# Kernel tuning notes

Measured on AMD Instinct MI355X. Metric: run time of the kernel, lower is better.

## Reference

```python
import jax, jax.numpy as jnp
import numpy as np

D_MODEL = 256; N_HEADS = 8; N_LEVELS = 4; N_POINTS = 4; D_FFN = 1024
BS = 8; NQ = 100; NKPT = 17
LEVEL_SHAPES = [(160, 160), (80, 80), (40, 40), (20, 20)]  # (H, W) per level
LEN_V = sum(h * w for h, w in LEVEL_SHAPES)  # 34000


def layer_norm(x, g, b, eps=1e-5):
    m = x.mean(-1, keepdims=True)
    v = ((x - m) ** 2).mean(-1, keepdims=True)
    return (x - m) * jax.lax.rsqrt(v + eps) * g + b


def mha(q, k, v, Wqkv, bqkv, Wo, bo):
    # torch nn.MultiheadAttention, batch_first, eval mode (no dropout)
    d = q.shape[-1]; dh = d // N_HEADS
    def proj(x, W, b):
        return (x @ W.T + b).reshape(*x.shape[:-1], N_HEADS, dh)
    qp = proj(q, Wqkv[:d], bqkv[:d])
    kp = proj(k, Wqkv[d:2 * d], bqkv[d:2 * d])
    vp = proj(v, Wqkv[2 * d:], bqkv[2 * d:])
    att = jnp.einsum('bqhd,bkhd->bhqk', qp, kp) / jnp.sqrt(jnp.asarray(dh, q.dtype))
    att = jax.nn.softmax(att, -1)
    out = jnp.einsum('bhqk,bkhd->bqhd', att, vp).reshape(q.shape)
    return out @ Wo.T + bo


def bilinear_sample(val, loc, h, w):
    # val: (B, H, h*w, Dh); loc: (B, Lq, H, P, 2) normalized to [0,1]
    # matches F.grid_sample(align_corners=False, padding_mode='zeros') on grid 2*loc-1
    B, Lq, H, P, _ = loc.shape
    px = loc[..., 0] * w - 0.5
    py = loc[..., 1] * h - 0.5
    x0f = jnp.floor(px); y0f = jnp.floor(py)
    lx = px - x0f; ly = py - y0f
    x0 = x0f.astype(jnp.int32); y0 = y0f.astype(jnp.int32)
    out = jnp.zeros((B, H, Lq, P, val.shape[-1]), val.dtype)
    for dx, dy, wt in ((0, 0, (1 - lx) * (1 - ly)), (1, 0, lx * (1 - ly)),
                       (0, 1, (1 - lx) * ly), (1, 1, lx * ly)):
        xi = x0 + dx; yi = y0 + dy
        valid = ((xi >= 0) & (xi < w) & (yi >= 0) & (yi < h)).astype(val.dtype)
        idx = jnp.clip(yi, 0, h - 1) * w + jnp.clip(xi, 0, w - 1)  # (B,Lq,H,P)
        idx = idx.transpose(0, 2, 1, 3).reshape(B, H, Lq * P)
        g = jnp.take_along_axis(val, idx[..., None], axis=2).reshape(B, H, Lq, P, -1)
        out = out + g * (wt * valid).transpose(0, 2, 1, 3)[..., None]
    return out  # (B, H, Lq, P, Dh)


def ms_deform_attn(query, ref_points, memory, off_W, off_b, aw_W, aw_b,
                   val_W, val_b, outp_W, outp_b):
    B, Lq, _ = query.shape
    dh = D_MODEL // N_HEADS
    value = (memory @ val_W.T + val_b).reshape(B, LEN_V, N_HEADS, dh)
    off = (query @ off_W.T + off_b).reshape(B, Lq, N_HEADS, N_LEVELS, N_POINTS, 2)
    aw = (query @ aw_W.T + aw_b).reshape(B, Lq, N_HEADS, N_LEVELS * N_POINTS)
    aw = jax.nn.softmax(aw, -1).reshape(B, Lq, N_HEADS, N_LEVELS, N_POINTS)
    normalizer = jnp.array([[w, h] for h, w in LEVEL_SHAPES], dtype=query.dtype)  # (L,2) as (W,H)
    loc = ref_points[:, :, None, :, None, :] + off / normalizer[None, None, None, :, None, :]
    out = jnp.zeros((B, Lq, N_HEADS, dh), query.dtype)
    start = 0
    for l, (h, w) in enumerate(LEVEL_SHAPES):
        vl = value[:, start:start + h * w].transpose(0, 2, 1, 3)  # (B,H,hw,Dh)
        s = bilinear_sample(vl, loc[:, :, :, l], h, w)            # (B,H,Lq,P,Dh)
        out = out + jnp.einsum('bhqpd,bqhp->bqhd', s, aw[:, :, :, l])
        start += h * w
    return out.reshape(B, Lq, D_MODEL) @ outp_W.T + outp_b


def setup_inputs() -> dict:
    key = jax.random.key(0)
    ks = iter(jax.random.split(key, 40))
    d = D_MODEL
    def w(shape, s=0.02):
        return jax.random.normal(next(ks), shape, jnp.float32) * s
    inp = {
        'tgt_pose': jax.random.normal(next(ks), (BS, NQ, NKPT, d), jnp.float32),
        'tgt_pose_query_pos': jax.random.normal(next(ks), (BS, NQ, NKPT, d), jnp.float32),
        'tgt_pose_reference_points': jax.random.uniform(next(ks), (BS, NQ * NKPT, N_LEVELS, 2), jnp.float32),
        'memory': jax.random.normal(next(ks), (BS, LEN_V, d), jnp.float32),
        'win_Wqkv': w((3 * d, d)), 'win_bqkv': jnp.zeros((3 * d,), jnp.float32),
        'win_Wo': w((d, d)), 'win_bo': jnp.zeros((d,), jnp.float32),
        'win_ng': jnp.ones((d,), jnp.float32), 'win_nb': jnp.zeros((d,), jnp.float32),
        'acr_Wqkv': w((3 * d, d)), 'acr_bqkv': jnp.zeros((3 * d,), jnp.float32),
        'acr_Wo': w((d, d)), 'acr_bo': jnp.zeros((d,), jnp.float32),
        'acr_ng': jnp.ones((d,), jnp.float32), 'acr_nb': jnp.zeros((d,), jnp.float32),
        'off_W': w((N_HEADS * N_LEVELS * N_POINTS * 2, d)),
        'off_b': jax.random.uniform(next(ks), (N_HEADS * N_LEVELS * N_POINTS * 2,), jnp.float32, -1.0, 1.0),
        'aw_W': w((N_HEADS * N_LEVELS * N_POINTS, d)), 'aw_b': jnp.zeros((N_HEADS * N_LEVELS * N_POINTS,), jnp.float32),
        'val_W': w((d, d)), 'val_b': jnp.zeros((d,), jnp.float32),
        'outp_W': w((d, d)), 'outp_b': jnp.zeros((d,), jnp.float32),
        'gate_W': w((2 * d, 2 * d)), 'gate_b': jnp.zeros((2 * d,), jnp.float32),
        'gate_ng': jnp.ones((d,), jnp.float32), 'gate_nb': jnp.zeros((d,), jnp.float32),
        'ffn_W1': w((D_FFN, d)), 'ffn_b1': jnp.zeros((D_FFN,), jnp.float32),
        'ffn_W2': w((d, D_FFN)), 'ffn_b2': jnp.zeros((d,), jnp.float32),
        'n2_g': jnp.ones((d,), jnp.float32), 'n2_b': jnp.zeros((d,), jnp.float32),
        'memory_spatial_shapes': jnp.array(LEVEL_SHAPES, jnp.int32),
    }
    return inp


def reference(tgt_pose, tgt_pose_query_pos, tgt_pose_reference_points, memory,
              win_Wqkv, win_bqkv, win_Wo, win_bo, win_ng, win_nb,
              acr_Wqkv, acr_bqkv, acr_Wo, acr_bo, acr_ng, acr_nb,
              off_W, off_b, aw_W, aw_b, val_W, val_b, outp_W, outp_b,
              gate_W, gate_b, gate_ng, gate_nb,
              ffn_W1, ffn_b1, ffn_W2, ffn_b2, n2_g, n2_b,
              memory_spatial_shapes):
    bs, nq, K, d = tgt_pose.shape
    # with_pos_embed mutates tgt_pose in place in the torch code -> residual includes pos
    tgt = tgt_pose + tgt_pose_query_pos
    # within-attention over keypoints of each query
    x = tgt.reshape(bs * nq, K, d)
    t2 = mha(x, x, x, win_Wqkv, win_bqkv, win_Wo, win_bo).reshape(bs, nq, K, d)
    tgt = layer_norm(tgt + t2, win_ng, win_nb)
    # across-attention over queries for each keypoint
    xk = tgt.transpose(0, 2, 1, 3).reshape(bs * K, nq, d)
    t2 = mha(xk, xk, xk, acr_Wqkv, acr_bqkv, acr_Wo, acr_bo)
    tgt = layer_norm(xk + t2, acr_ng, acr_nb).reshape(bs, K, nq, d).transpose(0, 2, 1, 3)
    # second in-place pos add before deformable cross-attn (also feeds gateway)
    tgt_q = tgt + tgt_pose_query_pos
    t2 = ms_deform_attn(tgt_q.reshape(bs, nq * K, d), tgt_pose_reference_points, memory,
                        off_W, off_b, aw_W, aw_b, val_W, val_b, outp_W, outp_b)
    t2 = t2.reshape(bs, nq, K, d)
    # Gate
    g = jax.nn.sigmoid(jnp.concatenate([tgt_q, t2], -1) @ gate_W.T + gate_b)
    g1, g2 = jnp.split(g, 2, -1)
    tgt = layer_norm(g1 * tgt_q + g2 * t2, gate_ng, gate_nb)
    # FFN
    h = jax.nn.relu(tgt @ ffn_W1.T + ffn_b1)
    tgt = tgt + h @ ffn_W2.T + ffn_b2
    tgt = layer_norm(jnp.clip(tgt, -65504.0, 65504.0), n2_g, n2_b)
    return tgt
```

## Files before the change

kernel.cpp:

```cpp
#include <hip/hip_runtime.h>
#include <hip/hip_bf16.h>

#define NH 8
#define BS_ 8
#define NQ_ 100
#define NK_ 17
#define LQ 1700
#define T_TOK 13600
#define LEN_VV 34000

typedef __attribute__((ext_vector_type(8))) short short8v;
typedef __attribute__((ext_vector_type(8))) __bf16 bf16x8;
typedef __attribute__((ext_vector_type(4))) float f32x4;

__device__ __forceinline__ float wave_sum(float v){
#pragma unroll
  for (int m = 32; m; m >>= 1) v += __shfl_xor(v, m, 64);
  return v;
}
__device__ __forceinline__ short f2bf(float f){
  __hip_bfloat16 h = __float2bfloat16(f);
  return *reinterpret_cast<short*>(&h);
}
__device__ __forceinline__ float bf2f(short s){
  return __uint_as_float(((uint)(unsigned short)s) << 16);
}

template<int EPI, int ADDA, int SWZ>
__global__ __launch_bounds__(256) void mgemm_k(const float* __restrict__ A,
                                               const float* __restrict__ A2,
                                               const float* __restrict__ W,
                                               const float* __restrict__ bias,
                                               __hip_bfloat16* __restrict__ Cb,
                                               int M, int N, int K, int nbx){
  __shared__ short sh[128 * 136];
  short* As = sh;
  short* Ws = sh + 128 * 64;
  int j;
  if (SWZ){
    int total = gridDim.x;
    int q = total >> 3, r = total & 7;
    int x = blockIdx.x & 7, k = blockIdx.x >> 3;
    j = (x < r) ? x * (q + 1) + k : r * (q + 1) + (x - r) * q + k;
  } else {
    j = blockIdx.x;
  }
  const int tid = threadIdx.x;
  const int bm = (j / nbx) * 128, bn = (j % nbx) * 128;
  const int wave = tid >> 6, lane = tid & 63;
  const int wm = (wave >> 1) * 64, wn = (wave & 1) * 64;
  const int s = tid & 7;
  const int row0 = tid >> 3;
  f32x4 acc[4][4] = {};
  const int lrow = lane & 15, lk = lane >> 4;

  float4 ra[8], rw[8];
#pragma unroll
  for (int i = 0; i < 4; i++){
    int row = row0 + i * 32;
    int gr = bm + row;
    float4 z = make_float4(0.f, 0.f, 0.f, 0.f);
    if (gr < M){
      const float* p = A + (size_t)gr * K + s * 8;
      float4 x0 = ((const float4*)p)[0], x1 = ((const float4*)p)[1];
      if (ADDA){
        const float* q2 = A2 + (size_t)gr * K + s * 8;
        float4 y0 = ((const float4*)q2)[0], y1 = ((const float4*)q2)[1];
        x0.x+=y0.x; x0.y+=y0.y; x0.z+=y0.z; x0.w+=y0.w;
        x1.x+=y1.x; x1.y+=y1.y; x1.z+=y1.z; x1.w+=y1.w;
      }
      ra[2 * i] = x0; ra[2 * i + 1] = x1;
    } else { ra[2 * i] = z; ra[2 * i + 1] = z; }
    const float* q = W + (size_t)(bn + row) * K + s * 8;
    rw[2 * i] = ((const float4*)q)[0]; rw[2 * i + 1] = ((const float4*)q)[1];
  }

  for (int k0 = 0; k0 < K; k0 += 64){
#pragma unroll
    for (int i = 0; i < 4; i++){
      int row = row0 + i * 32;
      int sw = ((s ^ (row & 7)) << 3) + row * 64;
      float4 a0 = ra[2 * i], a1 = ra[2 * i + 1];
      short8v v;
      v[0]=f2bf(a0.x); v[1]=f2bf(a0.y); v[2]=f2bf(a0.z); v[3]=f2bf(a0.w);
      v[4]=f2bf(a1.x); v[5]=f2bf(a1.y); v[6]=f2bf(a1.z); v[7]=f2bf(a1.w);
      *(short8v*)&As[sw] = v;
      a0 = rw[2 * i]; a1 = rw[2 * i + 1];
      short8v u;
      u[0]=f2bf(a0.x); u[1]=f2bf(a0.y); u[2]=f2bf(a0.z); u[3]=f2bf(a0.w);
      u[4]=f2bf(a1.x); u[5]=f2bf(a1.y); u[6]=f2bf(a1.z); u[7]=f2bf(a1.w);
      *(short8v*)&Ws[sw] = u;
    }
    __syncthreads();
    if (k0 + 64 < K){
#pragma unroll
      for (int i = 0; i < 4; i++){
        int row = row0 + i * 32;
        int gr = bm + row;
        float4 z = make_float4(0.f, 0.f, 0.f, 0.f);
        if (gr < M){
          const float* p = A + (size_t)gr * K + k0 + 64 + s * 8;
          float4 x0 = ((const float4*)p)[0], x1 = ((const float4*)p)[1];
          if (ADDA){
            const float* q2 = A2 + (size_t)gr * K + k0 + 64 + s * 8;
            float4 y0 = ((const float4*)q2)[0], y1 = ((const float4*)q2)[1];
            x0.x+=y0.x; x0.y+=y0.y; x0.z+=y0.z; x0.w+=y0.w;
            x1.x+=y1.x; x1.y+=y1.y; x1.z+=y1.z; x1.w+=y1.w;
          }
          ra[2 * i] = x0; ra[2 * i + 1] = x1;
        } else { ra[2 * i] = z; ra[2 * i + 1] = z; }
        const float* q = W + (size_t)(bn + row) * K + k0 + 64 + s * 8;
        rw[2 * i] = ((const float4*)q)[0]; rw[2 * i + 1] = ((const float4*)q)[1];
      }
    }
#pragma unroll
    for (int ks = 0; ks < 2; ks++){
      short8v af[4], bw[4];
      int slot = ks * 4 + lk;
#pragma unroll
      for (int m = 0; m < 4; m++){
        int r = wm + m * 16 + lrow;
        af[m] = *(const short8v*)&As[r * 64 + ((slot ^ (r & 7)) << 3)];
      }
#pragma unroll
      for (int n = 0; n < 4; n++){
        int r = wn + n * 16 + lrow;
        bw[n] = *(const short8v*)&Ws[r * 64 + ((slot ^ (r & 7)) << 3)];
      }
#pragma unroll
      for (int m = 0; m < 4; m++)
#pragma unroll
        for (int n = 0; n < 4; n++)
          acc[m][n] = __builtin_amdgcn_mfma_f32_16x16x32_bf16(
              __builtin_bit_cast(bf16x8, af[m]),
              __builtin_bit_cast(bf16x8, bw[n]), acc[m][n], 0, 0, 0);
    }
    __syncthreads();
  }
  const int STR = 136;
#pragma unroll
  for (int n = 0; n < 4; n++){
    int col = wn + n * 16 + lrow;
    float bsv = bias[bn + col];
#pragma unroll
    for (int m = 0; m < 4; m++){
#pragma unroll
      for (int i = 0; i < 4; i++){
        int row = wm + m * 16 + lk * 4 + i;
        float c = acc[m][n][i] + bsv;
        if (EPI == 1) c = fmaxf(c, 0.f);
        sh[row * STR + col] = f2bf(c);
      }
    }
  }
  __syncthreads();
#pragma unroll
  for (int it = 0; it < 8; it++){
    int r = it * 16 + (tid >> 4);
    int chunk = tid & 15;
    if (bm + r < M){
      uint4 v = *(const uint4*)((const char*)sh + r * 272 + chunk * 16);
      *(uint4*)((char*)Cb + ((size_t)(bm + r) * N + bn) * 2 + chunk * 16) = v;
    }
  }
}

template<int EPI, int OUTB, int INB, int DUALA>
__global__ __launch_bounds__(256) void g64_k(const void* __restrict__ Av,
                                             const void* __restrict__ A1v,
                                             const float* __restrict__ W0,
                                             const float* __restrict__ W1,
                                             int NSPLIT,
                                             const float* __restrict__ bias0,
                                             const float* __restrict__ bias1,
                                             const float* __restrict__ RES,
                                             float* __restrict__ Cf,
                                             __hip_bfloat16* __restrict__ Cb,
                                             int M, int N, int K, int sA){
  __shared__ short sh64[2 * 64 * 64];
  short* As = sh64;
  short* Ws = sh64 + 64 * 64;
  const int tid = threadIdx.x;
  const int bn = blockIdx.x * 64, bm = blockIdx.y * 64;
  const int wave = tid >> 6, lane = tid & 63;
  const int wm = (wave >> 1) * 32, wn = (wave & 1) * 32;
  const int s = tid & 7, row0 = tid >> 3;
  const int lrow = lane & 15, lk = lane >> 4;
  f32x4 acc[2][2] = {};

  for (int k0 = 0; k0 < K; k0 += 64){
#pragma unroll
    for (int i = 0; i < 2; i++){
      int row = row0 + i * 32;
      int sw = ((s ^ (row & 7)) << 3) + row * 64;
      short8v v = {};
      int gr = bm + row;
      if (gr < M){
        if (INB){
          v = *(const short8v*)((const short*)Av + (size_t)gr * sA + k0 + s * 8);
        } else {
          const float* Ap;
          if (DUALA) Ap = (k0 < 256) ? (const float*)Av + (size_t)gr * 256 + k0
                                     : (const float*)A1v + (size_t)gr * 256 + (k0 - 256);
          else Ap = (const float*)Av + (size_t)gr * sA + k0;
          float4 a0 = ((const float4*)(Ap + s * 8))[0];
          float4 a1 = ((const float4*)(Ap + s * 8))[1];
          v[0]=f2bf(a0.x); v[1]=f2bf(a0.y); v[2]=f2bf(a0.z); v[3]=f2bf(a0.w);
          v[4]=f2bf(a1.x); v[5]=f2bf(a1.y); v[6]=f2bf(a1.z); v[7]=f2bf(a1.w);
        }
      }
      *(short8v*)&As[sw] = v;
      int wr = bn + row;
      const float* Wp = (wr < NSPLIT) ? W0 + (size_t)wr * K + k0
                                      : W1 + (size_t)(wr - NSPLIT) * K + k0;
      float4 b0 = ((const float4*)(Wp + s * 8))[0];
      float4 b1 = ((const float4*)(Wp + s * 8))[1];
      short8v u;
      u[0]=f2bf(b0.x); u[1]=f2bf(b0.y); u[2]=f2bf(b0.z); u[3]=f2bf(b0.w);
      u[4]=f2bf(b1.x); u[5]=f2bf(b1.y); u[6]=f2bf(b1.z); u[7]=f2bf(b1.w);
      *(short8v*)&Ws[sw] = u;
    }
    __syncthreads();
#pragma unroll
    for (int ks = 0; ks < 2; ks++){
      int slot = ks * 4 + lk;
      short8v af[2], bw[2];
#pragma unroll
      for (int m = 0; m < 2; m++){
        int r = wm + m * 16 + lrow;
        af[m] = *(const short8v*)&As[r * 64 + ((slot ^ (r & 7)) << 3)];
      }
#pragma unroll
      for (int n = 0; n < 2; n++){
        int r = wn + n * 16 + lrow;
        bw[n] = *(const short8v*)&Ws[r * 64 + ((slot ^ (r & 7)) << 3)];
      }
#pragma unroll
      for (int m = 0; m < 2; m++)
#pragma unroll
        for (int n = 0; n < 2; n++)
          acc[m][n] = __builtin_amdgcn_mfma_f32_16x16x32_bf16(
              __builtin_bit_cast(bf16x8, af[m]),
              __builtin_bit_cast(bf16x8, bw[n]), acc[m][n], 0, 0, 0);
    }
    __syncthreads();
  }
  if (OUTB){
    const int STR = 72;
#pragma unroll
    for (int n = 0; n < 2; n++){
      int col = wn + n * 16 + lrow;
      int gc = bn + col;
      float bsv = (gc < NSPLIT) ? bias0[gc] : bias1[gc - NSPLIT];
#pragma unroll
      for (int m = 0; m < 2; m++){
#pragma unroll
        for (int i = 0; i < 4; i++){
          int row = wm + m * 16 + lk * 4 + i;
          float c = acc[m][n][i] + bsv;
          if (EPI == 1) c = fmaxf(c, 0.f);
          if (EPI == 2) c = 1.f / (1.f + expf(-c));
          sh64[row * STR + col] = f2bf(c);
        }
      }
    }
    __syncthreads();
#pragma unroll
    for (int it = 0; it < 2; it++){
      int r = it * 32 + (tid >> 3);
      int chunk = tid & 7;
      if (bm + r < M){
        uint4 v = *(const uint4*)((const char*)sh64 + r * 144 + chunk * 16);
        *(uint4*)((char*)Cb + ((size_t)(bm + r) * N + bn) * 2 + chunk * 16) = v;
      }
    }
  } else {
#pragma unroll
    for (int n = 0; n < 2; n++){
      int gc = bn + wn + n * 16 + lrow;
      float bsv = (gc < NSPLIT) ? bias0[gc] : bias1[gc - NSPLIT];
#pragma unroll
      for (int m = 0; m < 2; m++){
#pragma unroll
        for (int i = 0; i < 4; i++){
          int row = bm + wm + m * 16 + lk * 4 + i;
          if (row >= M) continue;
          float c = acc[m][n][i] + bsv;
          if (EPI == 1) c = fmaxf(c, 0.f);
          if (EPI == 2) c = 1.f / (1.f + expf(-c));
          if (EPI == 3) c += RES[(size_t)row * N + gc];
          Cf[(size_t)row * N + gc] = c;
        }
      }
    }
  }
}

template<int SITE>
__global__ __launch_bounds__(512) void gln_k(const short* __restrict__ Abf,
                                             const float* __restrict__ W,
                                             const float* __restrict__ bias,
                                             const float* __restrict__ r0,
                                             const float* __restrict__ r1,
                                             const float* __restrict__ g,
                                             const float* __restrict__ be,
                                             float* __restrict__ out,
                                             int M, int K){
  __shared__ short As[64 * 64];
  __shared__ short Ws[256 * 64];
  __shared__ float part[64][4][2];
  __shared__ float stats[64][2];
  const int tid = threadIdx.x;
  const int bm = blockIdx.x * 64;
  const int wave = tid >> 6, lane = tid & 63;
  const int wm = (wave >> 2) * 32, wn = (wave & 3) * 64;
  const int s = tid & 7, row0 = tid >> 3;
  const int lrow = lane & 15, lk = lane >> 4;
  f32x4 acc[2][4] = {};

  short8v pa = {};
  { int gr = bm + row0; if (gr < M) pa = *(const short8v*)(Abf + (size_t)gr * K + s * 8); }
  float4 pw[8];
#pragma unroll
  for (int i = 0; i < 4; i++){
    const float* wp = W + (size_t)(row0 + i * 64) * K + s * 8;
    pw[2 * i] = ((const float4*)wp)[0]; pw[2 * i + 1] = ((const float4*)wp)[1];
  }

  for (int k0 = 0; k0 < K; k0 += 64){
    *(short8v*)&As[row0 * 64 + ((s ^ (row0 & 7)) << 3)] = pa;
#pragma unroll
    for (int i = 0; i < 4; i++){
      int row = row0 + i * 64;
      float4 b0 = pw[2 * i], b1 = pw[2 * i + 1];
      short8v u;
      u[0]=f2bf(b0.x); u[1]=f2bf(b0.y); u[2]=f2bf(b0.z); u[3]=f2bf(b0.w);
      u[4]=f2bf(b1.x); u[5]=f2bf(b1.y); u[6]=f2bf(b1.z); u[7]=f2bf(b1.w);
      *(short8v*)&Ws[row * 64 + ((s ^ (row & 7)) << 3)] = u;
    }
    __syncthreads();
    if (k0 + 64 < K){
      int gr = bm + row0;
      pa = (short8v){};
      if (gr < M) pa = *(const short8v*)(Abf + (size_t)gr * K + k0 + 64 + s * 8);
#pragma unroll
      for (int i = 0; i < 4; i++){
        const float* wp = W + (size_t)(row0 + i * 64) * K + k0 + 64 + s * 8;
        pw[2 * i] = ((const float4*)wp)[0]; pw[2 * i + 1] = ((const float4*)wp)[1];
      }
    }
#pragma unroll
    for (int ks = 0; ks < 2; ks++){
      int slot = ks * 4 + lk;
      short8v af[2], bw[4];
#pragma unroll
      for (int m = 0; m < 2; m++){
        int r = wm + m * 16 + lrow;
        af[m] = *(const short8v*)&As[r * 64 + ((slot ^ (r & 7)) << 3)];
      }
#pragma unroll
      for (int n = 0; n < 4; n++){
        int r = wn + n * 16 + lrow;
        bw[n] = *(const short8v*)&Ws[r * 64 + ((slot ^ (r & 7)) << 3)];
      }
#pragma unroll
      for (int m = 0; m < 2; m++)
#pragma unroll
        for (int n = 0; n < 4; n++)
          acc[m][n] = __builtin_amdgcn_mfma_f32_16x16x32_bf16(
              __builtin_bit_cast(bf16x8, af[m]),
              __builtin_bit_cast(bf16x8, bw[n]), acc[m][n], 0, 0, 0);
    }
    __syncthreads();
  }

#pragma unroll
  for (int m = 0; m < 2; m++){
#pragma unroll
    for (int i = 0; i < 4; i++){
      int row = wm + m * 16 + lk * 4 + i;
      int grow = bm + row;
      float s1 = 0.f, s2 = 0.f;
      if (grow < M){
#pragma unroll
        for (int n = 0; n < 4; n++){
          int col = wn + n * 16 + lrow;
          float x = acc[m][n][i] + bias[col] + r0[(size_t)grow * 256 + col];
          if (SITE == 0) x += r1[(size_t)grow * 256 + col];
          if (SITE == 2) x = fminf(fmaxf(x, -65504.f), 65504.f);
          acc[m][n][i] = x;
          s1 += x; s2 += x * x;
        }
      }
#pragma unroll
      for (int msk = 1; msk <= 8; msk <<= 1){
        s1 += __shfl_xor(s1, msk, 64);
        s2 += __shfl_xor(s2, msk, 64);
      }
      if (lrow == 0){ part[row][wave & 3][0] = s1; part[row][wave & 3][1] = s2; }
    }
  }
  __syncthreads();
  if (tid < 64){
    float s1 = part[tid][0][0] + part[tid][1][0] + part[tid][2][0] + part[tid][3][0];
    float s2 = part[tid][0][1] + part[tid][1][1] + part[tid][2][1] + part[tid][3][1];
    float mean = s1 * (1.f / 256.f);
    float var = s2 * (1.f / 256.f) - mean * mean;
    stats[tid][0] = mean;
    stats[tid][1] = rsqrtf(fmaxf(var, 0.f) + 1e-5f);
  }
  __syncthreads();
#pragma unroll
  for (int m = 0; m < 2; m++){
#pragma unroll
    for (int i = 0; i < 4; i++){
      int row = wm + m * 16 + lk * 4 + i;
      int grow = bm + row;
      if (grow >= M) continue;
      float mean = stats[row][0], rstd = stats[row][1];
      size_t orow = grow;
      if (SITE == 0){
        int bi = grow / LQ; int rem = grow % LQ; int q = rem / NK_; int kk = rem % NK_;
        orow = (size_t)bi * LQ + kk * NQ_ + q;
      }
      if (SITE == 1){
        int bi = grow / LQ; int rem = grow % LQ; int kk = rem / NQ_; int q = rem % NQ_;
        orow = (size_t)bi * LQ + q * NK_ + kk;
      }
#pragma unroll
      for (int n = 0; n < 4; n++){
        int col = wn + n * 16 + lrow;
        float o = (acc[m][n][i] - mean) * rstd * g[col] + be[col];
        if (SITE == 1) o += r1[orow * 256 + col];
        out[orow * 256 + col] = o;
      }
    }
  }
}

template<int TP, int NSPL>
__global__ __launch_bounds__(256) void mha_mfma_k(const short* __restrict__ qkv,
                                                  __hip_bfloat16* __restrict__ out, int S){
  constexpr int MT = TP / 16;
  constexpr int KSTEPS = (TP + 31) / 32;
  constexpr int KS32 = KSTEPS * 32;
  constexpr int VSTRB = (KS32 == 128) ? 256 : 128;
  constexpr int CH = (MT + NSPL - 1) / NSPL;
  __shared__ short QK[2][TP][64];
  __shared__ short Vt[2][32][VSTRB / 2];
  __shared__ float Sc[2][16][128];
  __shared__ float rinv[2][16];

  const int tid = threadIdx.x;
  const int bid = blockIdx.x;
  const int batch = bid / (4 * NSPL);
  const int rem = bid % (4 * NSPL);
  const int hp = rem / NSPL;
  const int half = rem % NSPL;
  const int mtlo = half * CH;
  const int mthi = (mtlo + CH < MT) ? (mtlo + CH) : MT;
  const int wave = tid >> 6, lane = tid & 63;
  const int hh = wave >> 1, wsub = wave & 1;
  const int lrow = lane & 15, lk = lane >> 4;
  const float scale = 0.17677669529663687f;
  const size_t qbase = (size_t)batch * S * 768;

  for (int idx = tid; idx < 2 * TP * 4; idx += 256){
    int h2 = idx >= TP * 4;
    int rm = idx - h2 * TP * 4;
    int j = rm >> 2, s = rm & 3;
    int h = hp * 2 + h2;
    short8v qv = {}, kv = {};
    if (j < S){
      const short* p = qkv + qbase + (size_t)j * 768 + h * 32 + s * 8;
      qv = *(const short8v*)p;
      kv = *(const short8v*)(p + 256);
    }
    *(short8v*)&QK[h2][j][(s ^ (j & 7)) << 3] = qv;
    *(short8v*)&QK[h2][j][((s + 4) ^ (j & 7)) << 3] = kv;
  }
  for (int idx = tid; idx < 2 * KS32 * 4; idx += 256){
    int h2 = idx >= KS32 * 4;
    int rm = idx - h2 * KS32 * 4;
    int j = rm >> 2, e8 = rm & 3;
    int h = hp * 2 + h2;
    short8v v = {};
    if (j < S) v = *(const short8v*)(qkv + qbase + (size_t)j * 768 + h * 32 + 512 + e8 * 8);
#pragma unroll
    for (int c = 0; c < 8; c++){
      int e = e8 * 8 + c;
      char* pb = (char*)&Vt[h2][0][0] + e * VSTRB + (((j >> 3) ^ (e & 7)) << 4) + ((j & 7) << 1);
      *(short*)pb = v[c];
    }
  }
  __syncthreads();

  for (int mt = mtlo; mt < mthi; mt++){
    for (int nt = wsub; nt < MT; nt += 2){
      int ar = mt * 16 + lrow;
      short8v aq = *(const short8v*)&QK[hh][ar][(lk ^ (ar & 7)) << 3];
      int br = nt * 16 + lrow;
      short8v bk = *(const short8v*)&QK[hh][br][((lk + 4) ^ (br & 7)) << 3];
      f32x4 z = {};
      f32x4 d = __builtin_amdgcn_mfma_f32_16x16x32_bf16(
          __builtin_bit_cast(bf16x8, aq), __builtin_bit_cast(bf16x8, bk), z, 0, 0, 0);
#pragma unroll
      for (int i = 0; i < 4; i++){
        int rr = lk * 4 + i;
        int c = nt * 16 + lrow;
        Sc[hh][rr][(((c >> 2) ^ (rr & 7)) << 2) + (c & 3)] = d[i] * scale;
      }
    }
    __syncthreads();
    if (wsub == 0){
      int rr = lane >> 2, p = lane & 3;
      int grow = mt * 16 + rr;
      int Seff = (grow < S) ? S : 0;
      float mx = -1e30f;
#pragma unroll
      for (int m = 0; m < KSTEPS; m++){
        int j = p + 4 * m;
#pragma unroll
        for (int hf = 0; hf < 2; hf++){
          int ls = 2 * j + hf;
          float4 v = *(const float4*)&Sc[hh][rr][(ls ^ (rr & 7)) << 2];
          int c0 = ls * 4;
          mx = fmaxf(mx, (c0 + 0 < Seff) ? v.x : -1e30f);
          mx = fmaxf(mx, (c0 + 1 < Seff) ? v.y : -1e30f);
          mx = fmaxf(mx, (c0 + 2 < Seff) ? v.z : -1e30f);
          mx = fmaxf(mx, (c0 + 3 < Seff) ? v.w : -1e30f);
        }
      }
      mx = fmaxf(mx, __shfl_xor(mx, 1, 64));
      mx = fmaxf(mx, __shfl_xor(mx, 2, 64));
      float sum = 0.f;
#pragma unroll
      for (int m = 0; m < KSTEPS; m++){
        int j = p + 4 * m;
        float ev[8];
#pragma unroll
        for (int hf = 0; hf < 2; hf++){
          int ls = 2 * j + hf;
          float4 v = *(const float4*)&Sc[hh][rr][(ls ^ (rr & 7)) << 2];
          int c0 = ls * 4;
          ev[hf * 4 + 0] = (c0 + 0 < Seff) ? __expf(v.x - mx) : 0.f;
          ev[hf * 4 + 1] = (c0 + 1 < Seff) ? __expf(v.y - mx) : 0.f;
          ev[hf * 4 + 2] = (c0 + 2 < Seff) ? __expf(v.z - mx) : 0.f;
          ev[hf * 4 + 3] = (c0 + 3 < Seff) ? __expf(v.w - mx) : 0.f;
        }
        short8v pb;
#pragma unroll
        for (int q2 = 0; q2 < 8; q2++){ pb[q2] = f2bf(ev[q2]); sum += ev[q2]; }
        *(short8v*)((char*)&Sc[hh][rr][0] + ((j ^ (rr & 7)) << 4)) = pb;
      }
      sum += __shfl_xor(sum, 1, 64);
      sum += __shfl_xor(sum, 2, 64);
      if (p == 0) rinv[hh][rr] = (sum > 0.f) ? 1.f / sum : 0.f;
    }
    __syncthreads();
    {
      int nt2 = wsub;
      f32x4 acc = {};
#pragma unroll
      for (int ks = 0; ks < KSTEPS; ks++){
        int slot = ks * 4 + lk;
        short8v ap = *(const short8v*)((const char*)&Sc[hh][lrow][0] + ((slot ^ (lrow & 7)) << 4));
        int e = nt2 * 16 + lrow;
        short8v bv = *(const short8v*)((const char*)&Vt[hh][0][0] + e * VSTRB + ((slot ^ (e & 7)) << 4));
        acc = __builtin_amdgcn_mfma_f32_16x16x32_bf16(
            __builtin_bit_cast(bf16x8, ap), __builtin_bit_cast(bf16x8, bv), acc, 0, 0, 0);
      }
      int h = hp * 2 + hh;
#pragma unroll
      for (int i = 0; i < 4; i++){
        int row = mt * 16 + lk * 4 + i;
        if (row < S){
          float rv = rinv[hh][lk * 4 + i];
          out[((size_t)batch * S + row) * 256 + h * 32 + nt2 * 16 + lrow] =
              __float2bfloat16(acc[i] * rv);
        }
      }
    }
    __syncthreads();
  }
}

__global__ __launch_bounds__(64) void gate_ln_k(const short* __restrict__ G,
                                                const float* __restrict__ aq,
                                                const float* __restrict__ t2,
                                                const float* __restrict__ g,
                                                const float* __restrict__ be,
                                                float* __restrict__ out){
  int r = blockIdx.x;
  int lane = threadIdx.x;
  const short* gp = G + (size_t)r * 512 + lane * 4;
  float g1v[4], g2v[4];
#pragma unroll
  for (int i = 0; i < 4; i++){ g1v[i] = bf2f(gp[i]); g2v[i] = bf2f(gp[256 + i]); }
  float4 xa = *(const float4*)(aq + (size_t)r * 256 + lane * 4);
  float4 xt = *(const float4*)(t2 + (size_t)r * 256 + lane * 4);
  float x[4] = { g1v[0] * xa.x + g2v[0] * xt.x, g1v[1] * xa.y + g2v[1] * xt.y,
                 g1v[2] * xa.z + g2v[2] * xt.z, g1v[3] * xa.w + g2v[3] * xt.w };
  float s = x[0] + x[1] + x[2] + x[3];
  s = wave_sum(s);
  float mean = s * (1.f / 256.f);
  float sq = 0.f;
#pragma unroll
  for (int i = 0; i < 4; i++){ float d = x[i] - mean; sq += d * d; }
  float var = wave_sum(sq) * (1.f / 256.f);
  float rstd = rsqrtf(var + 1e-5f);
  float4 gg = *(const float4*)(g + lane * 4);
  float4 bb = *(const float4*)(be + lane * 4);
  float4 o;
  o.x = (x[0] - mean) * rstd * gg.x + bb.x;
  o.y = (x[1] - mean) * rstd * gg.y + bb.y;
  o.z = (x[2] - mean) * rstd * gg.z + bb.z;
  o.w = (x[3] - mean) * rstd * gg.w + bb.w;
  *(float4*)(out + (size_t)r * 256 + lane * 4) = o;
}

__global__ __launch_bounds__(256) void deform_k(const __hip_bfloat16* __restrict__ val,
                                                const float* __restrict__ offaw,
                                                const float* __restrict__ ref,
                                                unsigned int* __restrict__ outb){
  __shared__ uint2 meta[32][16][4];
  const int tid = threadIdx.x;
  const int t0 = blockIdx.x * 4;
  {
    int g = tid >> 3;
    int pair = tid & 7;
    int lt = g >> 3, h = g & 7;
    int t = t0 + lt;
    int b = t / LQ;
    int p0 = pair * 2;
    int l = p0 >> 2;
    const int starts[4] = {0, 25600, 32000, 33600};
    const int HS[4] = {160, 80, 40, 20};
    int w = HS[l];
    const float* ap = offaw + (size_t)t * 384 + 256 + h * 16;
    float a0 = ap[p0];
    float a1 = ap[p0 + 1];
    float mx = fmaxf(a0, a1);
#pragma unroll
    for (int m = 1; m <= 4; m <<= 1) mx = fmaxf(mx, __shfl_xor(mx, m, 64));
    float e0 = expf(a0 - mx), e1 = expf(a1 - mx);
    float s = e0 + e1;
#pragma unroll
    for (int m = 1; m <= 4; m <<= 1) s += __shfl_xor(s, m, 64);
    float inv = 1.f / s;
    float rx = ref[((size_t)t * 4 + l) * 2 + 0];
    float ry = ref[((size_t)t * 4 + l) * 2 + 1];
    float4 ov = *(const float4*)(offaw + (size_t)t * 384 + h * 32 + l * 8 + p0 * 2);
    int vbase = (b * LEN_VV + starts[l]) * 128 + h * 16;
#pragma unroll
    for (int pp = 0; pp < 2; pp++){
      float wgt = (pp ? e1 : e0) * inv;
      float px = rx * w + (pp ? ov.z : ov.x) - 0.5f;
      float py = ry * w + (pp ? ov.w : ov.y) - 0.5f;
      float x0f = floorf(px), y0f = floorf(py);
      float lx = px - x0f, ly = py - y0f;
      int x0 = (int)x0f, y0 = (int)y0f;
#pragma unroll
      for (int c = 0; c < 4; c++){
        int dx = c & 1, dy = c >> 1;
        int xi = x0 + dx, yi = y0 + dy;
        bool ok = (xi >= 0) & (xi < w) & (yi >= 0) & (yi < w);
        float cw = ok ? wgt * (dx ? lx : 1.f - lx) * (dy ? ly : 1.f - ly) : 0.f;
        uint idx = ok ? (uint)(vbase + (yi * w + xi) * 128) : 0u;
        uint2 m2; m2.x = idx; m2.y = __float_as_uint(cw);
        meta[g][p0 + pp][c] = m2;
      }
    }
  }
  __syncthreads();
  const uint2* V2 = (const uint2*)val;
  int sg = tid >> 3, lane8 = tid & 7;
  int lt = sg >> 3, h = sg & 7;
  int t = t0 + lt;
  float a0 = 0.f, a1 = 0.f, a2 = 0.f, a3 = 0.f;
#pragma unroll 4
  for (int c = 0; c < 64; c++){
    uint2 mw = meta[sg][c >> 2][c & 3];
    float wv = __uint_as_float(mw.y);
    uint2 v = V2[(size_t)(mw.x >> 1) + lane8];
    a0 += wv * __uint_as_float(v.x << 16);
    a1 += wv * __uint_as_float(v.x & 0xffff0000u);
    a2 += wv * __uint_as_float(v.y << 16);
    a3 += wv * __uint_as_float(v.y & 0xffff0000u);
  }
  uint2 u;
  u.x = ((uint)(unsigned short)f2bf(a1) << 16) | (uint)(unsigned short)f2bf(a0);
  u.y = ((uint)(unsigned short)f2bf(a3) << 16) | (uint)(unsigned short)f2bf(a2);
  ((uint2*)outb)[((size_t)t * 256 + h * 32) / 4 + lane8] = u;
}

extern "C" void kernel_launch(void* const* d_in, const int* in_sizes, int n_in,
                              void* d_out, int out_size, void* d_ws, size_t ws_size,
                              hipStream_t stream){
  const float* tgt_pose = (const float*)d_in[0];
  const float* qpos     = (const float*)d_in[1];
  const float* refp     = (const float*)d_in[2];
  const float* memory   = (const float*)d_in[3];
  const float* win_Wqkv = (const float*)d_in[4];
  const float* win_bqkv = (const float*)d_in[5];
  const float* win_Wo   = (const float*)d_in[6];
  const float* win_bo   = (const float*)d_in[7];
  const float* win_ng   = (const float*)d_in[8];
  const float* win_nb   = (const float*)d_in[9];
  const float* acr_Wqkv = (const float*)d_in[10];
  const float* acr_bqkv = (const float*)d_in[11];
  const float* acr_Wo   = (const float*)d_in[12];
  const float* acr_bo   = (const float*)d_in[13];
  const float* acr_ng   = (const float*)d_in[14];
  const float* acr_nb   = (const float*)d_in[15];
  const float* off_W    = (const float*)d_in[16];
  const float* off_b    = (const float*)d_in[17];
  const float* aw_W     = (const float*)d_in[18];
  const float* aw_b     = (const float*)d_in[19];
  const float* val_W    = (const float*)d_in[20];
  const float* val_b    = (const float*)d_in[21];
  const float* outp_W   = (const float*)d_in[22];
  const float* outp_b   = (const float*)d_in[23];
  const float* gate_W   = (const float*)d_in[24];
  const float* gate_b   = (const float*)d_in[25];
  const float* gate_ng  = (const float*)d_in[26];
  const float* gate_nb  = (const float*)d_in[27];
  const float* ffn_W1   = (const float*)d_in[28];
  const float* ffn_b1   = (const float*)d_in[29];
  const float* ffn_W2   = (const float*)d_in[30];
  const float* ffn_b2   = (const float*)d_in[31];
  const float* n2_g     = (const float*)d_in[32];
  const float* n2_b     = (const float*)d_in[33];

  float* out = (float*)d_out;
  char* ws = (char*)d_ws;
  const size_t TB = (size_t)T_TOK * 256 * 4;
  float* B0 = (float*)(ws);
  float* B1 = (float*)(ws + TB);
  float* B2 = (float*)(ws + 2 * TB);
  float* B3 = (float*)(ws + 3 * TB);
  char* p = ws + 4 * TB;
  short* Qb = (short*)p;                 p += (size_t)T_TOK * 768 * 2;
  short* ABF = (short*)p;                p += (size_t)T_TOK * 256 * 2;
  float* OFFAW = (float*)p;              p += (size_t)T_TOK * 384 * 4;
  short* Gb = (short*)p;                 p += (size_t)T_TOK * 512 * 2;
  char* Vregion = p;
  __hip_bfloat16* V = (__hip_bfloat16*)Vregion;
  short* FF = (short*)Vregion;

  const int GM128 = (T_TOK + 127) / 128;
  const int GM64  = (T_TOK + 63) / 64;
  const int BIG = 1 << 30;

  mgemm_k<0,0,1><<<2 * 2125, 256, 0, stream>>>(memory, nullptr, val_W, val_b, V, BS_ * LEN_VV, 256, 256, 2);
  mgemm_k<0,1,0><<<6 * GM128, 256, 0, stream>>>(tgt_pose, qpos, win_Wqkv, win_bqkv, (__hip_bfloat16*)Qb, T_TOK, 768, 256, 6);
  mha_mfma_k<32,1><<<800 * 4, 256, 0, stream>>>(Qb, (__hip_bfloat16*)ABF, 17);
  gln_k<0><<<GM64, 512, 0, stream>>>(ABF, win_Wo, win_bo, tgt_pose, qpos, win_ng, win_nb, B1, T_TOK, 256);
  mgemm_k<0,0,0><<<6 * GM128, 256, 0, stream>>>(B1, nullptr, acr_Wqkv, acr_bqkv, (__hip_bfloat16*)Qb, T_TOK, 768, 256, 6);
  mha_mfma_k<112,2><<<136 * 8, 256, 0, stream>>>(Qb, (__hip_bfloat16*)ABF, 100);
  gln_k<1><<<GM64, 512, 0, stream>>>(ABF, acr_Wo, acr_bo, B1, qpos, acr_ng, acr_nb, B0, T_TOK, 256);
  g64_k<0,0,0,0><<<dim3(6, GM64), 256, 0, stream>>>(B0, nullptr, off_W, aw_W, 256, off_b, aw_b, nullptr, OFFAW, nullptr, T_TOK, 384, 256, 256);
  deform_k<<<T_TOK / 4, 256, 0, stream>>>(V, OFFAW, refp, (unsigned int*)ABF);
  g64_k<0,0,1,0><<<dim3(4, GM64), 256, 0, stream>>>(ABF, nullptr, outp_W, outp_W, BIG, outp_b, outp_b, nullptr, B3, nullptr, T_TOK, 256, 256, 256);
  g64_k<2,1,0,1><<<dim3(8, GM64), 256, 0, stream>>>(B0, B3, gate_W, gate_W, BIG, gate_b, gate_b, nullptr, nullptr, (__hip_bfloat16*)Gb, T_TOK, 512, 512, 256);
  gate_ln_k<<<T_TOK, 64, 0, stream>>>(Gb, B0, B3, gate_ng, gate_nb, B2);
  mgemm_k<1,0,0><<<8 * GM128, 256, 0, stream>>>(B2, nullptr, ffn_W1, ffn_b1, (__hip_bfloat16*)FF, T_TOK, 1024, 256, 8);
  gln_k<2><<<GM64, 512, 0, stream>>>(FF, ffn_W2, ffn_b2, B2, nullptr, n2_g, n2_b, out, T_TOK, 1024);
}
```

Baseline: 467.3 us.

## Fuse gate GEMM with sigmoid and LayerNorm; store intermediates as bf16

Replaces the separate gate GEMM and the per-row gate LayerNorm kernel with one kernel. That kernel computes the 512-wide gate projection from the concatenated bf16 inputs, applies the sigmoid into shared memory, then does the gated mix and LayerNorm in the same block. The post-cross-attention activation (tgt_q) and the deformable output projection are now written as bf16 instead of fp32, which cuts memory traffic and lets the offset GEMM read bf16 directly. The cost is lower precision in the residual path into the gate. The fused kernel also uses a large shared tile, about 72 KB, which may reduce occupancy, and it converts the weights to bf16 inside every block.

Measured after the change: 462.3 us. Within noise of the previous version (-1.1%).

```diff
diff --git a/kernel.cpp b/kernel.cpp
--- a/kernel.cpp
+++ b/kernel.cpp
@@ -13,11 +13,6 @@
 typedef __attribute__((ext_vector_type(8))) __bf16 bf16x8;
 typedef __attribute__((ext_vector_type(4))) float f32x4;
 
-__device__ __forceinline__ float wave_sum(float v){
-#pragma unroll
-  for (int m = 32; m; m >>= 1) v += __shfl_xor(v, m, 64);
-  return v;
-}
 __device__ __forceinline__ short f2bf(float f){
   __hip_bfloat16 h = __float2bfloat16(f);
   return *reinterpret_cast<short*>(&h);
@@ -296,7 +291,7 @@
   }
 }
 
-template<int SITE>
+template<int SITE, int OUTB>
 __global__ __launch_bounds__(512) void gln_k(const short* __restrict__ Abf,
                                              const float* __restrict__ W,
                                              const float* __restrict__ bias,
@@ -304,7 +299,7 @@
                                              const float* __restrict__ r1,
                                              const float* __restrict__ g,
                                              const float* __restrict__ be,
-                                             float* __restrict__ out,
+                                             void* __restrict__ outv,
                                              int M, int K){
   __shared__ short As[64 * 64];
   __shared__ short Ws[256 * 64];
@@ -432,7 +427,134 @@
         int col = wn + n * 16 + lrow;
         float o = (acc[m][n][i] - mean) * rstd * g[col] + be[col];
         if (SITE == 1) o += r1[orow * 256 + col];
-        out[orow * 256 + col] = o;
+        if (OUTB) ((short*)outv)[orow * 256 + col] = f2bf(o);
+        else      ((float*)outv)[orow * 256 + col] = o;
+      }
+    }
+  }
+}
+
+__global__ __launch_bounds__(512) void gateln_k(const short* __restrict__ TQ,
+                                                const short* __restrict__ T2,
+                                                const float* __restrict__ W,
+                                                const float* __restrict__ bias,
+                                                const float* __restrict__ g,
+                                                const float* __restrict__ be,
+                                                float* __restrict__ out, int M){
+  __shared__ short sh[64 * 64 + 512 * 64];
+  short* As = sh;
+  short* Ws = sh + 64 * 64;
+  const int tid = threadIdx.x;
+  const int bm = blockIdx.x * 64;
+  const int wave = tid >> 6, lane = tid & 63;
+  const int wm = (wave >> 2) * 32, wn = (wave & 3) * 128;
+  const int s = tid & 7, row0 = tid >> 3;
+  const int lrow = lane & 15, lk = lane >> 4;
+  f32x4 acc[2][8] = {};
+
+  for (int k0 = 0; k0 < 512; k0 += 64){
+    {
+      short8v v = {};
+      int gr = bm + row0;
+      if (gr < M){
+        v = (k0 < 256) ? *(const short8v*)(TQ + (size_t)gr * 256 + k0 + s * 8)
+                       : *(const short8v*)(T2 + (size_t)gr * 256 + (k0 - 256) + s * 8);
+      }
+      *(short8v*)&As[row0 * 64 + ((s ^ (row0 & 7)) << 3)] = v;
+    }
+#pragma unroll
+    for (int i = 0; i < 8; i++){
+      int row = row0 + i * 64;
+      const float* wp = W + (size_t)row * 512 + k0 + s * 8;
+      float4 b0 = ((const float4*)wp)[0], b1 = ((const float4*)wp)[1];
+      short8v u;
+      u[0]=f2bf(b0.x); u[1]=f2bf(b0.y); u[2]=f2bf(b0.z); u[3]=f2bf(b0.w);
+      u[4]=f2bf(b1.x); u[5]=f2bf(b1.y); u[6]=f2bf(b1.z); u[7]=f2bf(b1.w);
+      *(short8v*)&Ws[row * 64 + ((s ^ (row & 7)) << 3)] = u;
+    }
+    __syncthreads();
+#pragma unroll
+    for (int ks = 0; ks < 2; ks++){
+      int slot = ks * 4 + lk;
+      short8v af[2], bw[8];
+#pragma unroll
+      for (int m = 0; m < 2; m++){
+        int r = wm + m * 16 + lrow;
+        af[m] = *(const short8v*)&As[r * 64 + ((slot ^ (r & 7)) << 3)];
+      }
+#pragma unroll
+      for (int n = 0; n < 8; n++){
+        int r = wn + n * 16 + lrow;
+        bw[n] = *(const short8v*)&Ws[r * 64 + ((slot ^ (r & 7)) << 3)];
+      }
+#pragma unroll
+      for (int m = 0; m < 2; m++)
+#pragma unroll
+        for (int n = 0; n < 8; n++)
+          acc[m][n] = __builtin_amdgcn_mfma_f32_16x16x32_bf16(
+              __builtin_bit_cast(bf16x8, af[m]),
+              __builtin_bit_cast(bf16x8, bw[n]), acc[m][n], 0, 0, 0);
+    }
+    __syncthreads();
+  }
+  short* gb = sh;
+  const int GSTR = 520;
+#pragma unroll
+  for (int n = 0; n < 8; n++){
+    int col = wn + n * 16 + lrow;
+    float bsv = bias[col];
+#pragma unroll
+    for (int m = 0; m < 2; m++){
+#pragma unroll
+      for (int i = 0; i < 4; i++){
+        int row = wm + m * 16 + lk * 4 + i;
+        float c = acc[m][n][i] + bsv;
+        gb[row * GSTR + col] = f2bf(1.f / (1.f + __expf(-c)));
+      }
+    }
+  }
+  __syncthreads();
+  {
+    int row = tid >> 3, cg = tid & 7;
+    int grow = bm + row;
+    float x[32];
+    float s1 = 0.f, s2 = 0.f;
+    if (grow < M){
+#pragma unroll
+      for (int jv = 0; jv < 4; jv++){
+        int c0 = cg * 32 + jv * 8;
+        short8v aqv = *(const short8v*)(TQ + (size_t)grow * 256 + c0);
+        short8v t2v = *(const short8v*)(T2 + (size_t)grow * 256 + c0);
+#pragma unroll
+        for (int jj = 0; jj < 8; jj++){
+          float g1 = bf2f(gb[row * GSTR + c0 + jj]);
+          float g2 = bf2f(gb[row * GSTR + 256 + c0 + jj]);
+          float xv = g1 * bf2f(aqv[jj]) + g2 * bf2f(t2v[jj]);
+          x[jv * 8 + jj] = xv; s1 += xv; s2 += xv * xv;
+        }
+      }
+    }
+    s1 += __shfl_xor(s1, 1, 64); s2 += __shfl_xor(s2, 1, 64);
+    s1 += __shfl_xor(s1, 2, 64); s2 += __shfl_xor(s2, 2, 64);
+    s1 += __shfl_xor(s1, 4, 64); s2 += __shfl_xor(s2, 4, 64);
+    float mean = s1 * (1.f / 256.f);
+    float var = s2 * (1.f / 256.f) - mean * mean;
+    float rstd = rsqrtf(fmaxf(var, 0.f) + 1e-5f);
+    if (grow < M){
+#pragma unroll
+      for (int jv = 0; jv < 4; jv++){
+        int c0 = cg * 32 + jv * 8;
+        float4 o0, o1;
+        float* po = (float*)&o0;
+#pragma unroll
+        for (int jj = 0; jj < 8; jj++){
+          int c = c0 + jj;
+          float o = (x[jv * 8 + jj] - mean) * rstd * g[c] + be[c];
+          if (jj < 4) ((float*)&o0)[jj] = o; else ((float*)&o1)[jj - 4] = o;
+        }
+        (void)po;
+        *(float4*)(out + (size_t)grow * 256 + c0) = o0;
+        *(float4*)(out + (size_t)grow * 256 + c0 + 4) = o1;
       }
     }
   }
@@ -583,40 +705,6 @@
     }
     __syncthreads();
   }
-}
-
-__global__ __launch_bounds__(64) void gate_ln_k(const short* __restrict__ G,
-                                                const float* __restrict__ aq,
-                                                const float* __restrict__ t2,
-                                                const float* __restrict__ g,
-                                                const float* __restrict__ be,
-                                                float* __restrict__ out){
-  int r = blockIdx.x;
-  int lane = threadIdx.x;
-  const short* gp = G + (size_t)r * 512 + lane * 4;
-  float g1v[4], g2v[4];
-#pragma unroll
-  for (int i = 0; i < 4; i++){ g1v[i] = bf2f(gp[i]); g2v[i] = bf2f(gp[256 + i]); }
-  float4 xa = *(const float4*)(aq + (size_t)r * 256 + lane * 4);
-  float4 xt = *(const float4*)(t2 + (size_t)r * 256 + lane * 4);
-  float x[4] = { g1v[0] * xa.x + g2v[0] * xt.x, g1v[1] * xa.y + g2v[1] * xt.y,
-                 g1v[2] * xa.z + g2v[2] * xt.z, g1v[3] * xa.w + g2v[3] * xt.w };
-  float s = x[0] + x[1] + x[2] + x[3];
-  s = wave_sum(s);
-  float mean = s * (1.f / 256.f);
-  float sq = 0.f;
-#pragma unroll
-  for (int i = 0; i < 4; i++){ float d = x[i] - mean; sq += d * d; }
-  float var = wave_sum(sq) * (1.f / 256.f);
-  float rstd = rsqrtf(var + 1e-5f);
-  float4 gg = *(const float4*)(g + lane * 4);
-  float4 bb = *(const float4*)(be + lane * 4);
-  float4 o;
-  o.x = (x[0] - mean) * rstd * gg.x + bb.x;
-  o.y = (x[1] - mean) * rstd * gg.y + bb.y;
-  o.z = (x[2] - mean) * rstd * gg.z + bb.z;
-  o.w = (x[3] - mean) * rstd * gg.w + bb.w;
-  *(float4*)(out + (size_t)r * 256 + lane * 4) = o;
 }
 
 __global__ __launch_bounds__(256) void deform_k(const __hip_bfloat16* __restrict__ val,
@@ -735,15 +823,14 @@
   float* out = (float*)d_out;
   char* ws = (char*)d_ws;
   const size_t TB = (size_t)T_TOK * 256 * 4;
-  float* B0 = (float*)(ws);
-  float* B1 = (float*)(ws + TB);
-  float* B2 = (float*)(ws + 2 * TB);
-  float* B3 = (float*)(ws + 3 * TB);
-  char* p = ws + 4 * TB;
-  short* Qb = (short*)p;                 p += (size_t)T_TOK * 768 * 2;
-  short* ABF = (short*)p;                p += (size_t)T_TOK * 256 * 2;
-  float* OFFAW = (float*)p;              p += (size_t)T_TOK * 384 * 4;
-  short* Gb = (short*)p;                 p += (size_t)T_TOK * 512 * 2;
+  float* B1 = (float*)(ws);
+  float* B2 = (float*)(ws + TB);
+  char* p = ws + 2 * TB;
+  short* Qb  = (short*)p;  p += (size_t)T_TOK * 768 * 2;
+  short* ABF = (short*)p;  p += (size_t)T_TOK * 256 * 2;
+  short* TQb = (short*)p;  p += (size_t)T_TOK * 256 * 2;
+  short* T2b = (short*)p;  p += (size_t)T_TOK * 256 * 2;
+  float* OFFAW = (float*)p; p += (size_t)T_TOK * 384 * 4;
   char* Vregion = p;
   __hip_bfloat16* V = (__hip_bfloat16*)Vregion;
   short* FF = (short*)Vregion;
@@ -755,15 +842,14 @@
   mgemm_k<0,0,1><<<2 * 2125, 256, 0, stream>>>(memory, nullptr, val_W, val_b, V, BS_ * LEN_VV, 256, 256, 2);
   mgemm_k<0,1,0><<<6 * GM128, 256, 0, stream>>>(tgt_pose, qpos, win_Wqkv, win_bqkv, (__hip_bfloat16*)Qb, T_TOK, 768, 256, 6);
   mha_mfma_k<32,1><<<800 * 4, 256, 0, stream>>>(Qb, (__hip_bfloat16*)ABF, 17);
-  gln_k<0><<<GM64, 512, 0, stream>>>(ABF, win_Wo, win_bo, tgt_pose, qpos, win_ng, win_nb, B1, T_TOK, 256);
+  gln_k<0,0><<<GM64, 512, 0, stream>>>(ABF, win_Wo, win_bo, tgt_pose, qpos, win_ng, win_nb, B1, T_TOK, 256);
   mgemm_k<0,0,0><<<6 * GM128, 256, 0, stream>>>(B1, nullptr, acr_Wqkv, acr_bqkv, (__hip_bfloat16*)Qb, T_TOK, 768, 256, 6);
   mha_mfma_k<112,2><<<136 * 8, 256, 0, stream>>>(Qb, (__hip_bfloat16*)ABF, 100);
-  gln_k<1><<<GM64, 512, 0, stream>>>(ABF, acr_Wo, acr_bo, B1, qpos, acr_ng, acr_nb, B0, T_TOK, 256);
-  g64_k<0,0,0,0><<<dim3(6, GM64), 256, 0, stream>>>(B0, nullptr, off_W, aw_W, 256, off_b, aw_b, nullptr, OFFAW, nullptr, T_TOK, 384, 256, 256);
+  gln_k<1,1><<<GM64, 512, 0, stream>>>(ABF, acr_Wo, acr_bo, B1, qpos, acr_ng, acr_nb, TQb, T_TOK, 256);
+  g64_k<0,0,1,0><<<dim3(6, GM64), 256, 0, stream>>>(TQb, nullptr, off_W, aw_W, 256, off_b, aw_b, nullptr, OFFAW, nullptr, T_TOK, 384, 256, 256);
   deform_k<<<T_TOK / 4, 256, 0, stream>>>(V, OFFAW, refp, (unsigned int*)ABF);
-  g64_k<0,0,1,0><<<dim3(4, GM64), 256, 0, stream>>>(ABF, nullptr, outp_W, outp_W, BIG, outp_b, outp_b, nullptr, B3, nullptr, T_TOK, 256, 256, 256);
-  g64_k<2,1,0,1><<<dim3(8, GM64), 256, 0, stream>>>(B0, B3, gate_W, gate_W, BIG, gate_b, gate_b, nullptr, nullptr, (__hip_bfloat16*)Gb, T_TOK, 512, 512, 256);
-  gate_ln_k<<<T_TOK, 64, 0, stream>>>(Gb, B0, B3, gate_ng, gate_nb, B2);
+  g64_k<0,1,1,0><<<dim3(4, GM64), 256, 0, stream>>>(ABF, nullptr, outp_W, outp_W, BIG, outp_b, outp_b, nullptr, nullptr, (__hip_bfloat16*)T2b, T_TOK, 256, 256, 256);
+  gateln_k<<<GM64, 512, 0, stream>>>(TQb, T2b, gate_W, gate_b, gate_ng, gate_nb, B2, T_TOK);
   mgemm_k<1,0,0><<<8 * GM128, 256, 0, stream>>>(B2, nullptr, ffn_W1, ffn_b1, (__hip_bfloat16*)FF, T_TOK, 1024, 256, 8);
-  gln_k<2><<<GM64, 512, 0, stream>>>(FF, ffn_W2, ffn_b2, B2, nullptr, n2_g, n2_b, out, T_TOK, 1024);
+  gln_k<2,0><<<GM64, 512, 0, stream>>>(FF, ffn_W2, ffn_b2, B2, nullptr, n2_g, n2_b, out, T_TOK, 1024);
 }
```
